# Optimization experiments

Hardware: AMD Instinct MI355X
Metric: run time of the kernel (lower is better)

## Reference

```python
import jax, jax.numpy as jnp
import numpy as np

K = 3
OUT_H, OUT_W = 32, 512
INVALID_DIST = 1e10  # stands in for filtering out zero points on the reference side


def _downsample(pc, out_H=OUT_H, out_W=OUT_W):
    # pc: [B, H, W, 3] -> [B, out_H, out_W, 3] via strided index selection
    B, H, W, _ = pc.shape
    sH, sW = H // out_H, W // out_W
    return pc[:, : out_H * sH : sH, : out_W * sW : sW, :]


def _batch_knn_mean(tgt, src):
    # tgt: [Nt, 3] reference points; src: [Ns, 3] query points.
    # move_zero_point filters points whose xyz are all zero; with fixed shapes we
    # emulate this by masking: invalid refs get huge distance (never selected in
    # top-k unless all refs invalid), invalid queries are excluded from the mean.
    valid_t = jnp.any(tgt != 0.0, axis=-1)  # [Nt]
    valid_s = jnp.any(src != 0.0, axis=-1)  # [Ns]
    # pairwise squared Euclidean distance [Ns, Nt]
    d2 = (
        jnp.sum(src * src, axis=-1)[:, None]
        + jnp.sum(tgt * tgt, axis=-1)[None, :]
        - 2.0 * (src @ tgt.T)
    )
    d = jnp.sqrt(jnp.maximum(d2, 0.0))  # KNN_CUDA returns Euclidean distance
    d = jnp.where(valid_t[None, :], d, INVALID_DIST)
    neg_topk, _ = jax.lax.top_k(-d, K)  # k smallest distances per query
    dk = -neg_topk  # [Ns, K]
    w = valid_s.astype(d.dtype)
    denom = K * jnp.maximum(jnp.sum(w), 1.0)
    return jnp.sum(dk * w[:, None]) / denom  # mean over valid query knn dists


def reference(source_pc, target_pc):
    # source_pc: [B, H, W, 3]; target_pc: [B, 3, H, W]
    B = source_pc.shape[0]
    tgt = _downsample(jnp.transpose(target_pc, (0, 2, 3, 1))).reshape(B, -1, 3)
    src = _downsample(source_pc).reshape(B, -1, 3)
    per_batch = jax.vmap(_batch_knn_mean)(tgt, src)  # [B]
    return jnp.mean(per_batch)


def setup_inputs() -> dict:
    key = jax.random.key(0)
    k1, k2 = jax.random.split(key)
    source_pc = jax.random.normal(k1, (2, 64, 2048, 3), dtype=jnp.float32)
    target_pc = jax.random.normal(k2, (2, 3, 64, 2048), dtype=jnp.float32)
    return {"source_pc": source_pc, "target_pc": target_pc}
```

## Files before the change

kernel.cpp:

```cpp
#include <hip/hip_runtime.h>
#include <math.h>

#define NB 2
#define NQ 16384
#define IN_H 64
#define IN_W 2048
#define BIG 1e30f
#define NQT (NB * NQ)
#define NG 4
#define NP (NG * 3)

typedef __bf16 bf16x8 __attribute__((ext_vector_type(8)));
typedef float f32x16 __attribute__((ext_vector_type(16)));

__device__ inline float med3(float a, float b, float c) {
    return __builtin_amdgcn_fmed3f(a, b, c);
}
#define INSERT3(B0, B1, B2, V)                    \
    do { float _v = (V);                          \
         (B2) = med3((B1), (B2), _v);             \
         (B1) = med3((B0), (B1), _v);             \
         (B0) = fminf((B0), _v); } while (0)

union PK { __bf16 h[8]; uint4 u; };

__global__ __launch_bounds__(256) void pack_kernel(
    const float* __restrict__ tgt_pc,
    uint4* __restrict__ packed,
    float4* __restrict__ tgt4,
    float* __restrict__ zws)
{
    if (blockIdx.x == 0 && threadIdx.x < 16) zws[threadIdx.x] = 0.f;

    int gid = blockIdx.x * 256 + threadIdx.x;
    int b = gid >> 14, t = gid & (NQ - 1);
    int oh = t >> 9, ow = t & 511;
    const size_t PL = (size_t)IN_H * IN_W;
    size_t base = ((size_t)(b * 3) * IN_H + oh * 2) * IN_W + ow * 4;
    float x = tgt_pc[base], y = tgt_pc[base + PL], z = tgt_pc[base + 2 * PL];
    bool valid = (x != 0.f) || (y != 0.f) || (z != 0.f);
    float ntx = x * x + y * y + z * z;
    float nt = valid ? ntx : BIG;
    float tx = valid ? -2.f * x : 0.f;
    float ty = valid ? -2.f * y : 0.f;
    float tz = valid ? -2.f * z : 0.f;

    __bf16 txh = (__bf16)tx, tyh = (__bf16)ty, tzh = (__bf16)tz;
    __bf16 txl = (__bf16)(tx - (float)txh);
    __bf16 tyl = (__bf16)(ty - (float)tyh);
    __bf16 tzl = (__bf16)(tz - (float)tzh);
    __bf16 nth = (__bf16)nt;
    __bf16 ntl = (__bf16)(nt - (float)nth);

    PK h0, h1;
    h0.h[0] = txh; h0.h[1] = tyh; h0.h[2] = tzh; h0.h[3] = txh;
    h0.h[4] = tyh; h0.h[5] = tzh; h0.h[6] = txl; h0.h[7] = tyl;
    h1.h[0] = tzl; h1.h[1] = nth; h1.h[2] = ntl; h1.h[3] = (__bf16)1.0f;
    h1.h[4] = (__bf16)1.0f; h1.h[5] = (__bf16)0.0f;
    h1.h[6] = (__bf16)0.0f; h1.h[7] = (__bf16)0.0f;

    int tile = t >> 5, m = t & 31;
    size_t o = (size_t)(b * 512 + tile) * 64 + m;
    packed[o]      = h0.u;
    packed[o + 32] = h1.u;

    tgt4[gid] = make_float4(valid ? x : 0.f, valid ? y : 0.f,
                            valid ? z : 0.f, valid ? ntx : 1e20f);
}

#define COMPUTE_TILE(U, IDX)                                                  \
    do {                                                                      \
        bf16x8 af = __builtin_bit_cast(bf16x8, (U));                          \
        f32x16 d = __builtin_amdgcn_mfma_f32_32x32x16_bf16(af, bq, zero, 0, 0, 0); \
        float m0 = fminf(fminf(d[0], d[1]), fminf(d[2], d[3]));               \
        float m1 = fminf(fminf(d[4], d[5]), fminf(d[6], d[7]));               \
        float m2 = fminf(fminf(d[8], d[9]), fminf(d[10], d[11]));             \
        float m3 = fminf(fminf(d[12], d[13]), fminf(d[14], d[15]));           \
        float m = fminf(fminf(m0, m1), fminf(m2, m3));                        \
        unsigned u = (__float_as_uint(m) & ~127u) | (unsigned)(IDX);          \
        float pv = __uint_as_float(u);                                        \
        if ((IDX) & 1) { INSERT3(c0b, c1b, c2b, pv); }                        \
        else           { INSERT3(c0a, c1a, c2a, pv); }                        \
    } while (0)

__global__ __launch_bounds__(256, 4) void knn_mfma(
    const float* __restrict__ src_pc,
    const uint4* __restrict__ packed,
    const float4* __restrict__ tgt4,
    float* __restrict__ partial)
{
    const int tid = threadIdx.x;
    const int lane = tid & 63;
    const int w = tid >> 6;
    int blk = blockIdx.x;
    int qt = blk & 127;
    int quarter = (blk >> 7) & 3;
    int b = blk >> 9;

    int n = lane & 31;
    int q = qt * 128 + w * 32 + n;
    size_t sbase = (((size_t)b * IN_H + (q >> 9) * 2) * IN_W + (q & 511) * 4) * 3;
    float sx = src_pc[sbase], sy = src_pc[sbase + 1], sz = src_pc[sbase + 2];
    float ns = sx * sx + sy * sy + sz * sz;
    __bf16 sxh = (__bf16)sx, syh = (__bf16)sy, szh = (__bf16)sz;
    __bf16 sxl = (__bf16)(sx - (float)sxh);
    __bf16 syl = (__bf16)(sy - (float)syh);
    __bf16 szl = (__bf16)(sz - (float)szh);
    __bf16 nsh = (__bf16)ns;
    __bf16 nsl = (__bf16)(ns - (float)nsh);
    bf16x8 bq;
    if ((lane >> 5) == 0) {
        bq[0] = sxh; bq[1] = syh; bq[2] = szh; bq[3] = sxl;
        bq[4] = syl; bq[5] = szl; bq[6] = sxh; bq[7] = syh;
    } else {
        bq[0] = szh; bq[1] = (__bf16)1.0f; bq[2] = (__bf16)1.0f; bq[3] = nsh;
        bq[4] = nsl; bq[5] = (__bf16)0.0f; bq[6] = (__bf16)0.0f; bq[7] = (__bf16)0.0f;
    }

    f32x16 zero;
    #pragma unroll
    for (int i = 0; i < 16; ++i) zero[i] = 0.f;

    float c0a = BIG, c1a = BIG, c2a = BIG;
    float c0b = BIG, c1b = BIG, c2b = BIG;

    const uint4* pkq = packed + (size_t)b * 32768 + (size_t)quarter * 8192 + lane;

    uint4 bufA[8], bufB[8];
    #pragma unroll
    for (int i = 0; i < 8; ++i) bufA[i] = pkq[i * 64];

    #pragma unroll
    for (int gg = 0; gg < 8; ++gg) {
        #pragma unroll
        for (int i = 0; i < 8; ++i) bufB[i] = pkq[((2 * gg + 1) * 8 + i) * 64];
        #pragma unroll
        for (int i = 0; i < 8; ++i) COMPUTE_TILE(bufA[i], 2 * gg * 8 + i);
        if (gg < 7) {
            #pragma unroll
            for (int i = 0; i < 8; ++i) bufA[i] = pkq[((2 * gg + 2) * 8 + i) * 64];
        }
        #pragma unroll
        for (int i = 0; i < 8; ++i) COMPUTE_TILE(bufB[i], (2 * gg + 1) * 8 + i);
    }

    INSERT3(c0a, c1a, c2a, c0b);
    INSERT3(c0a, c1a, c2a, c1b);
    INSERT3(c0a, c1a, c2a, c2b);

    int half = lane >> 5;
    int ti[3] = { (int)(__float_as_uint(c0a) & 127u),
                  (int)(__float_as_uint(c1a) & 127u),
                  (int)(__float_as_uint(c2a) & 127u) };
    float e0 = BIG, e1 = BIG, e2 = BIG;
    const float4* t4b = tgt4 + (size_t)b * NQ + (size_t)quarter * 4096;
    #pragma unroll
    for (int i = 0; i < 3; ++i) {
        int tbase = ti[i] * 32 + 4 * half;
        #pragma unroll
        for (int rr = 0; rr < 16; ++rr) {
            int row = (rr & 3) + 8 * (rr >> 2);
            float4 t4 = t4b[tbase + row];
            float dot = sx * t4.x;
            dot = fmaf(sy, t4.y, dot);
            dot = fmaf(sz, t4.z, dot);
            float d2 = fmaf(-2.f, dot, ns + t4.w);
            INSERT3(e0, e1, e2, d2);
        }
    }

    float f0 = __shfl_down(e0, 32, 64);
    float f1 = __shfl_down(e1, 32, 64);
    float f2 = __shfl_down(e2, 32, 64);
    if (lane < 32) {
        INSERT3(e0, e1, e2, f0);
        INSERT3(e0, e1, e2, f1);
        INSERT3(e0, e1, e2, f2);
        int gq = b * NQ + q;
        partial[(quarter * 3 + 0) * NQT + gq] = e0;
        partial[(quarter * 3 + 1) * NQT + gq] = e1;
        partial[(quarter * 3 + 2) * NQT + gq] = e2;
    }
}

__global__ __launch_bounds__(256) void merge_final(
    const float* __restrict__ partial,
    const float* __restrict__ src_pc,
    float* __restrict__ accum,
    int* __restrict__ done_cnt,
    float* __restrict__ out)
{
    int gid = blockIdx.x * 256 + threadIdx.x;
    int b = gid >> 14;
    int q = gid & (NQ - 1);

    float b0 = BIG, b1 = BIG, b2 = BIG;
    #pragma unroll
    for (int c = 0; c < NP; ++c) {
        float v = partial[c * NQT + gid];
        INSERT3(b0, b1, b2, v);
    }

    size_t base = (((size_t)b * IN_H + (q >> 9) * 2) * IN_W + (q & 511) * 4) * 3;
    float x = src_pc[base], y = src_pc[base + 1], z = src_pc[base + 2];
    float wt = ((x != 0.f) || (y != 0.f) || (z != 0.f)) ? 1.f : 0.f;

    float d = fminf(sqrtf(fmaxf(b0, 0.f)), 1e10f)
            + fminf(sqrtf(fmaxf(b1, 0.f)), 1e10f)
            + fminf(sqrtf(fmaxf(b2, 0.f)), 1e10f);
    float dsum = d * wt;

    #pragma unroll
    for (int off = 32; off > 0; off >>= 1) {
        dsum += __shfl_down(dsum, off, 64);
        wt   += __shfl_down(wt, off, 64);
    }
    __shared__ float sd[4], sw4[4];
    int lane = threadIdx.x & 63, wv = threadIdx.x >> 6;
    if (lane == 0) { sd[wv] = dsum; sw4[wv] = wt; }
    __syncthreads();
    if (threadIdx.x == 0) {
        atomicAdd(&accum[b * 2 + 0], sd[0] + sd[1] + sd[2] + sd[3]);
        atomicAdd(&accum[b * 2 + 1], sw4[0] + sw4[1] + sw4[2] + sw4[3]);
        __threadfence();
        int done = atomicAdd(done_cnt, 1);
        if (done == (int)gridDim.x - 1) {
            float s0 = atomicAdd(&accum[0], 0.f);
            float c0 = atomicAdd(&accum[1], 0.f);
            float s1 = atomicAdd(&accum[2], 0.f);
            float c1 = atomicAdd(&accum[3], 0.f);
            float r = s0 / (3.0f * fmaxf(c0, 1.0f))
                    + s1 / (3.0f * fmaxf(c1, 1.0f));
            out[0] = r / (float)NB;
        }
    }
}

extern "C" void kernel_launch(void* const* d_in, const int* in_sizes, int n_in,
                              void* d_out, int out_size, void* d_ws, size_t ws_size,
                              hipStream_t stream) {
    const float* src_pc = (const float*)d_in[0];
    const float* tgt_pc = (const float*)d_in[1];
    float* out = (float*)d_out;

    char* ws = (char*)d_ws;
    float*  accum   = (float*)ws;
    int*    done    = (int*)(ws + 32);
    float*  partial = (float*)(ws + 64);
    uint4*  packed  = (uint4*)(ws + 2097152);
    float4* tgt4    = (float4*)(ws + 3145728);

    pack_kernel<<<NQT / 256, 256, 0, stream>>>(tgt_pc, packed, tgt4, (float*)ws);
    knn_mfma<<<NB * NG * 128, 256, 0, stream>>>(src_pc, packed, tgt4, partial);
    merge_final<<<NQT / 256, 256, 0, stream>>>(partial, src_pc, accum, done, out);
}
```

Before: 108.4 us.

## Split target tiles across warps per query group and merge candidates via LDS

Each block now handles 32 queries, and its four warps each scan a different quarter of the target tiles (32 tiles each) instead of every warp scanning all 128 tiles for its own queries. Per-warp top-3 tile candidates are merged through shared memory, three warps each refine one candidate tile exactly, and warp 0 merges the results and writes partials. The aim is shorter per-warp dependency chains and more blocks (4x grid) for better latency hiding. The cost is two block barriers, some LDS traffic, a warp left idle during refinement, and recomputing the source loads in four times as many blocks.

```diff
diff --git a/kernel.cpp b/kernel.cpp
--- a/kernel.cpp
+++ b/kernel.cpp
@@ -77,7 +77,7 @@
         float m2 = fminf(fminf(d[8], d[9]), fminf(d[10], d[11]));             \
         float m3 = fminf(fminf(d[12], d[13]), fminf(d[14], d[15]));           \
         float m = fminf(fminf(m0, m1), fminf(m2, m3));                        \
-        unsigned u = (__float_as_uint(m) & ~127u) | (unsigned)(IDX);          \
+        unsigned u = (__float_as_uint(m) & ~127u) | wbase | (unsigned)(IDX);  \
         float pv = __uint_as_float(u);                                        \
         if ((IDX) & 1) { INSERT3(c0b, c1b, c2b, pv); }                        \
         else           { INSERT3(c0a, c1a, c2a, pv); }                        \
@@ -89,16 +89,19 @@
     const float4* __restrict__ tgt4,
     float* __restrict__ partial)
 {
+    __shared__ float lds_c[4][2][32][3];
+    __shared__ float lds_e[3][2][32][3];
     const int tid = threadIdx.x;
     const int lane = tid & 63;
     const int w = tid >> 6;
     int blk = blockIdx.x;
-    int qt = blk & 127;
-    int quarter = (blk >> 7) & 3;
-    int b = blk >> 9;
+    int qg = blk & 511;
+    int quarter = (blk >> 9) & 3;
+    int b = blk >> 11;
 
     int n = lane & 31;
-    int q = qt * 128 + w * 32 + n;
+    int half = lane >> 5;
+    int q = qg * 32 + n;
     size_t sbase = (((size_t)b * IN_H + (q >> 9) * 2) * IN_W + (q & 511) * 4) * 3;
     float sx = src_pc[sbase], sy = src_pc[sbase + 1], sz = src_pc[sbase + 2];
     float ns = sx * sx + sy * sy + sz * sz;
@@ -109,7 +112,7 @@
     __bf16 nsh = (__bf16)ns;
     __bf16 nsl = (__bf16)(ns - (float)nsh);
     bf16x8 bq;
-    if ((lane >> 5) == 0) {
+    if (half == 0) {
         bq[0] = sxh; bq[1] = syh; bq[2] = szh; bq[3] = sxl;
         bq[4] = syl; bq[5] = szl; bq[6] = sxh; bq[7] = syh;
     } else {
@@ -124,39 +127,51 @@
     float c0a = BIG, c1a = BIG, c2a = BIG;
     float c0b = BIG, c1b = BIG, c2b = BIG;
 
-    const uint4* pkq = packed + (size_t)b * 32768 + (size_t)quarter * 8192 + lane;
-
-    uint4 bufA[8], bufB[8];
-    #pragma unroll
-    for (int i = 0; i < 8; ++i) bufA[i] = pkq[i * 64];
-
-    #pragma unroll
-    for (int gg = 0; gg < 8; ++gg) {
-        #pragma unroll
-        for (int i = 0; i < 8; ++i) bufB[i] = pkq[((2 * gg + 1) * 8 + i) * 64];
-        #pragma unroll
-        for (int i = 0; i < 8; ++i) COMPUTE_TILE(bufA[i], 2 * gg * 8 + i);
-        if (gg < 7) {
+    unsigned wbase = (unsigned)(w << 5);
+    const uint4* pkq = packed + (size_t)b * 32768 + (size_t)quarter * 8192
+                              + (size_t)(w * 32) * 64 + lane;
+
+    uint4 bufA[4], bufB[4];
+    #pragma unroll
+    for (int i = 0; i < 4; ++i) bufA[i] = pkq[i * 64];
+
+    #pragma unroll
+    for (int gg = 0; gg < 4; ++gg) {
+        #pragma unroll
+        for (int i = 0; i < 4; ++i) bufB[i] = pkq[((2 * gg + 1) * 4 + i) * 64];
+        #pragma unroll
+        for (int i = 0; i < 4; ++i) COMPUTE_TILE(bufA[i], 2 * gg * 4 + i);
+        if (gg < 3) {
             #pragma unroll
-            for (int i = 0; i < 8; ++i) bufA[i] = pkq[((2 * gg + 2) * 8 + i) * 64];
-        }
-        #pragma unroll
-        for (int i = 0; i < 8; ++i) COMPUTE_TILE(bufB[i], (2 * gg + 1) * 8 + i);
+            for (int i = 0; i < 4; ++i) bufA[i] = pkq[((2 * gg + 2) * 4 + i) * 64];
+        }
+        #pragma unroll
+        for (int i = 0; i < 4; ++i) COMPUTE_TILE(bufB[i], (2 * gg + 1) * 4 + i);
     }
 
     INSERT3(c0a, c1a, c2a, c0b);
     INSERT3(c0a, c1a, c2a, c1b);
     INSERT3(c0a, c1a, c2a, c2b);
 
-    int half = lane >> 5;
-    int ti[3] = { (int)(__float_as_uint(c0a) & 127u),
-                  (int)(__float_as_uint(c1a) & 127u),
-                  (int)(__float_as_uint(c2a) & 127u) };
-    float e0 = BIG, e1 = BIG, e2 = BIG;
-    const float4* t4b = tgt4 + (size_t)b * NQ + (size_t)quarter * 4096;
-    #pragma unroll
-    for (int i = 0; i < 3; ++i) {
-        int tbase = ti[i] * 32 + 4 * half;
+    lds_c[w][half][n][0] = c0a;
+    lds_c[w][half][n][1] = c1a;
+    lds_c[w][half][n][2] = c2a;
+    __syncthreads();
+
+    float m0 = BIG, m1 = BIG, m2 = BIG;
+    #pragma unroll
+    for (int ww = 0; ww < 4; ++ww) {
+        INSERT3(m0, m1, m2, lds_c[ww][half][n][0]);
+        INSERT3(m0, m1, m2, lds_c[ww][half][n][1]);
+        INSERT3(m0, m1, m2, lds_c[ww][half][n][2]);
+    }
+
+    if (w < 3) {
+        float mw = (w == 0) ? m0 : ((w == 1) ? m1 : m2);
+        int tloc = (int)(__float_as_uint(mw) & 127u);
+        float e0 = BIG, e1 = BIG, e2 = BIG;
+        const float4* t4b = tgt4 + (size_t)b * NQ + (size_t)quarter * 4096;
+        int tbase = tloc * 32 + 4 * half;
         #pragma unroll
         for (int rr = 0; rr < 16; ++rr) {
             int row = (rr & 3) + 8 * (rr >> 2);
@@ -167,19 +182,32 @@
             float d2 = fmaf(-2.f, dot, ns + t4.w);
             INSERT3(e0, e1, e2, d2);
         }
-    }
-
-    float f0 = __shfl_down(e0, 32, 64);
-    float f1 = __shfl_down(e1, 32, 64);
-    float f2 = __shfl_down(e2, 32, 64);
-    if (lane < 32) {
-        INSERT3(e0, e1, e2, f0);
-        INSERT3(e0, e1, e2, f1);
-        INSERT3(e0, e1, e2, f2);
-        int gq = b * NQ + q;
-        partial[(quarter * 3 + 0) * NQT + gq] = e0;
-        partial[(quarter * 3 + 1) * NQT + gq] = e1;
-        partial[(quarter * 3 + 2) * NQT + gq] = e2;
+        lds_e[w][half][n][0] = e0;
+        lds_e[w][half][n][1] = e1;
+        lds_e[w][half][n][2] = e2;
+    }
+    __syncthreads();
+
+    if (w == 0) {
+        float e0 = BIG, e1 = BIG, e2 = BIG;
+        #pragma unroll
+        for (int ww = 0; ww < 3; ++ww) {
+            INSERT3(e0, e1, e2, lds_e[ww][half][n][0]);
+            INSERT3(e0, e1, e2, lds_e[ww][half][n][1]);
+            INSERT3(e0, e1, e2, lds_e[ww][half][n][2]);
+        }
+        float f0 = __shfl_down(e0, 32, 64);
+        float f1 = __shfl_down(e1, 32, 64);
+        float f2 = __shfl_down(e2, 32, 64);
+        if (lane < 32) {
+            INSERT3(e0, e1, e2, f0);
+            INSERT3(e0, e1, e2, f1);
+            INSERT3(e0, e1, e2, f2);
+            int gq = b * NQ + q;
+            partial[(quarter * 3 + 0) * NQT + gq] = e0;
+            partial[(quarter * 3 + 1) * NQT + gq] = e1;
+            partial[(quarter * 3 + 2) * NQT + gq] = e2;
+        }
     }
 }
 
@@ -251,6 +279,6 @@
     float4* tgt4    = (float4*)(ws + 3145728);
 
     pack_kernel<<<NQT / 256, 256, 0, stream>>>(tgt_pc, packed, tgt4, (float*)ws);
-    knn_mfma<<<NB * NG * 128, 256, 0, stream>>>(src_pc, packed, tgt4, partial);
+    knn_mfma<<<NB * NG * 512, 256, 0, stream>>>(src_pc, packed, tgt4, partial);
     merge_final<<<NQT / 256, 256, 0, stream>>>(partial, src_pc, accum, done, out);
 }
```

New measurement: 113.8 us. 5.0% more time.

## Fuse final merge into kNN kernel via last-arriving block counter

Applied to the files above, without the earlier changes.

Removes the separate merge kernel. Each kNN block atomically increments a per-query-tile counter, and the last of the four quarter blocks merges the partial top-3 lists and accumulates the weighted distance sums. This saves a kernel launch and the inter-kernel gap. The change also shrinks the double-buffered prefetch from 8 to 4 tiles per stage, which lowers register pressure but gives less latency hiding. The merge work now runs in the tail of the kNN grid, with half the threads of each merging block idle.

```diff
diff --git a/kernel.cpp b/kernel.cpp
--- a/kernel.cpp
+++ b/kernel.cpp
@@ -30,7 +30,10 @@
     float4* __restrict__ tgt4,
     float* __restrict__ zws)
 {
-    if (blockIdx.x == 0 && threadIdx.x < 16) zws[threadIdx.x] = 0.f;
+    if (blockIdx.x == 0) {
+        zws[threadIdx.x] = 0.f;
+        if (threadIdx.x < 32) zws[256 + threadIdx.x] = 0.f;
+    }
 
     int gid = blockIdx.x * 256 + threadIdx.x;
     int b = gid >> 14, t = gid & (NQ - 1);
@@ -83,11 +86,15 @@
         else           { INSERT3(c0a, c1a, c2a, pv); }                        \
     } while (0)
 
-__global__ __launch_bounds__(256, 4) void knn_mfma(
+__global__ __launch_bounds__(256, 4) void knn_merge(
     const float* __restrict__ src_pc,
     const uint4* __restrict__ packed,
     const float4* __restrict__ tgt4,
-    float* __restrict__ partial)
+    float* __restrict__ partial,
+    float* __restrict__ accum,
+    int* __restrict__ qcnt,
+    int* __restrict__ done_cnt,
+    float* __restrict__ out)
 {
     const int tid = threadIdx.x;
     const int lane = tid & 63;
@@ -126,22 +133,22 @@
 
     const uint4* pkq = packed + (size_t)b * 32768 + (size_t)quarter * 8192 + lane;
 
-    uint4 bufA[8], bufB[8];
-    #pragma unroll
-    for (int i = 0; i < 8; ++i) bufA[i] = pkq[i * 64];
-
-    #pragma unroll
-    for (int gg = 0; gg < 8; ++gg) {
-        #pragma unroll
-        for (int i = 0; i < 8; ++i) bufB[i] = pkq[((2 * gg + 1) * 8 + i) * 64];
-        #pragma unroll
-        for (int i = 0; i < 8; ++i) COMPUTE_TILE(bufA[i], 2 * gg * 8 + i);
-        if (gg < 7) {
+    uint4 bufA4[4], bufB4[4];
+    #pragma unroll
+    for (int i = 0; i < 4; ++i) bufA4[i] = pkq[i * 64];
+
+    #pragma unroll
+    for (int gg = 0; gg < 16; ++gg) {
+        #pragma unroll
+        for (int i = 0; i < 4; ++i) bufB4[i] = pkq[((2 * gg + 1) * 4 + i) * 64];
+        #pragma unroll
+        for (int i = 0; i < 4; ++i) COMPUTE_TILE(bufA4[i], 8 * gg + i);
+        if (gg < 15) {
             #pragma unroll
-            for (int i = 0; i < 8; ++i) bufA[i] = pkq[((2 * gg + 2) * 8 + i) * 64];
-        }
-        #pragma unroll
-        for (int i = 0; i < 8; ++i) COMPUTE_TILE(bufB[i], (2 * gg + 1) * 8 + i);
+            for (int i = 0; i < 4; ++i) bufA4[i] = pkq[((2 * gg + 2) * 4 + i) * 64];
+        }
+        #pragma unroll
+        for (int i = 0; i < 4; ++i) COMPUTE_TILE(bufB4[i], 8 * gg + 4 + i);
     }
 
     INSERT3(c0a, c1a, c2a, c0b);
@@ -181,57 +188,58 @@
         partial[(quarter * 3 + 1) * NQT + gq] = e1;
         partial[(quarter * 3 + 2) * NQT + gq] = e2;
     }
-}
-
-__global__ __launch_bounds__(256) void merge_final(
-    const float* __restrict__ partial,
-    const float* __restrict__ src_pc,
-    float* __restrict__ accum,
-    int* __restrict__ done_cnt,
-    float* __restrict__ out)
-{
-    int gid = blockIdx.x * 256 + threadIdx.x;
-    int b = gid >> 14;
-    int q = gid & (NQ - 1);
-
-    float b0 = BIG, b1 = BIG, b2 = BIG;
-    #pragma unroll
-    for (int c = 0; c < NP; ++c) {
-        float v = partial[c * NQT + gid];
-        INSERT3(b0, b1, b2, v);
-    }
-
-    size_t base = (((size_t)b * IN_H + (q >> 9) * 2) * IN_W + (q & 511) * 4) * 3;
-    float x = src_pc[base], y = src_pc[base + 1], z = src_pc[base + 2];
-    float wt = ((x != 0.f) || (y != 0.f) || (z != 0.f)) ? 1.f : 0.f;
-
-    float d = fminf(sqrtf(fmaxf(b0, 0.f)), 1e10f)
-            + fminf(sqrtf(fmaxf(b1, 0.f)), 1e10f)
-            + fminf(sqrtf(fmaxf(b2, 0.f)), 1e10f);
-    float dsum = d * wt;
-
-    #pragma unroll
-    for (int off = 32; off > 0; off >>= 1) {
-        dsum += __shfl_down(dsum, off, 64);
-        wt   += __shfl_down(wt, off, 64);
-    }
-    __shared__ float sd[4], sw4[4];
-    int lane = threadIdx.x & 63, wv = threadIdx.x >> 6;
-    if (lane == 0) { sd[wv] = dsum; sw4[wv] = wt; }
+
+    __shared__ int do_merge;
     __syncthreads();
-    if (threadIdx.x == 0) {
-        atomicAdd(&accum[b * 2 + 0], sd[0] + sd[1] + sd[2] + sd[3]);
-        atomicAdd(&accum[b * 2 + 1], sw4[0] + sw4[1] + sw4[2] + sw4[3]);
+    if (tid == 0) {
         __threadfence();
-        int done = atomicAdd(done_cnt, 1);
-        if (done == (int)gridDim.x - 1) {
-            float s0 = atomicAdd(&accum[0], 0.f);
-            float c0 = atomicAdd(&accum[1], 0.f);
-            float s1 = atomicAdd(&accum[2], 0.f);
-            float c1 = atomicAdd(&accum[3], 0.f);
-            float r = s0 / (3.0f * fmaxf(c0, 1.0f))
-                    + s1 / (3.0f * fmaxf(c1, 1.0f));
-            out[0] = r / (float)NB;
+        int old = atomicAdd(&qcnt[b * 128 + qt], 1);
+        do_merge = (old == NG - 1) ? 1 : 0;
+    }
+    __syncthreads();
+
+    if (do_merge) {
+        float dsum = 0.f, wt = 0.f;
+        if (tid < 128) {
+            int qq = qt * 128 + tid;
+            int gq = b * NQ + qq;
+            float b0 = BIG, b1 = BIG, b2 = BIG;
+            #pragma unroll
+            for (int c = 0; c < NP; ++c) {
+                float v = partial[c * NQT + gq];
+                INSERT3(b0, b1, b2, v);
+            }
+            size_t sb2 = (((size_t)b * IN_H + (qq >> 9) * 2) * IN_W
+                          + (qq & 511) * 4) * 3;
+            float x = src_pc[sb2], y = src_pc[sb2 + 1], z = src_pc[sb2 + 2];
+            wt = ((x != 0.f) || (y != 0.f) || (z != 0.f)) ? 1.f : 0.f;
+            float d = fminf(sqrtf(fmaxf(b0, 0.f)), 1e10f)
+                    + fminf(sqrtf(fmaxf(b1, 0.f)), 1e10f)
+                    + fminf(sqrtf(fmaxf(b2, 0.f)), 1e10f);
+            dsum = d * wt;
+        }
+        #pragma unroll
+        for (int off = 32; off > 0; off >>= 1) {
+            dsum += __shfl_down(dsum, off, 64);
+            wt   += __shfl_down(wt, off, 64);
+        }
+        __shared__ float sd[4], sw4[4];
+        if (lane == 0) { sd[w] = dsum; sw4[w] = wt; }
+        __syncthreads();
+        if (tid == 0) {
+            atomicAdd(&accum[b * 2 + 0], sd[0] + sd[1] + sd[2] + sd[3]);
+            atomicAdd(&accum[b * 2 + 1], sw4[0] + sw4[1] + sw4[2] + sw4[3]);
+            __threadfence();
+            int dd = atomicAdd(done_cnt, 1);
+            if (dd == NB * 128 - 1) {
+                float s0 = atomicAdd(&accum[0], 0.f);
+                float c0 = atomicAdd(&accum[1], 0.f);
+                float s1 = atomicAdd(&accum[2], 0.f);
+                float c1 = atomicAdd(&accum[3], 0.f);
+                float r = s0 / (3.0f * fmaxf(c0, 1.0f))
+                        + s1 / (3.0f * fmaxf(c1, 1.0f));
+                out[0] = r / (float)NB;
+            }
         }
     }
 }
@@ -246,11 +254,12 @@
     char* ws = (char*)d_ws;
     float*  accum   = (float*)ws;
     int*    done    = (int*)(ws + 32);
-    float*  partial = (float*)(ws + 64);
+    int*    qcnt    = (int*)(ws + 64);
+    float*  partial = (float*)(ws + 4096);
     uint4*  packed  = (uint4*)(ws + 2097152);
     float4* tgt4    = (float4*)(ws + 3145728);
 
     pack_kernel<<<NQT / 256, 256, 0, stream>>>(tgt_pc, packed, tgt4, (float*)ws);
-    knn_mfma<<<NB * NG * 128, 256, 0, stream>>>(src_pc, packed, tgt4, partial);
-    merge_final<<<NQT / 256, 256, 0, stream>>>(partial, src_pc, accum, done, out);
-}
+    knn_merge<<<NB * NG * 128, 256, 0, stream>>>(src_pc, packed, tgt4,
+                                                 partial, accum, qcnt, done, out);
+}
```

Result: slower. 129.1 us (+19.2%).
